# Optimization experiments

Measured on AMD Instinct MI355X. Metric: run time of the kernel, lower is better.

Reference implementation:

```python
import jax, jax.numpy as jnp
import numpy as np

D_MODEL = 1024
D_STATE = 16
D_CONV = 4
BATCH = 2
SEQ = 2048


def setup_inputs() -> dict:
    key = jax.random.key(0)
    ks = jax.random.split(key, 10)
    s = lambda fan_in: 1.0 / np.sqrt(fan_in)
    x = jax.random.normal(ks[0], (BATCH, SEQ, D_MODEL), dtype=jnp.float32)
    W_in = jax.random.normal(ks[1], (D_MODEL, 2 * D_MODEL), dtype=jnp.float32) * s(D_MODEL)
    conv_w = jax.random.normal(ks[2], (D_MODEL, D_CONV), dtype=jnp.float32) * s(D_CONV)
    conv_b = jax.random.normal(ks[3], (D_MODEL,), dtype=jnp.float32) * 0.01
    W_x = jax.random.normal(ks[4], (D_MODEL, 2 * D_STATE), dtype=jnp.float32) * s(D_MODEL)
    W_dt = jax.random.normal(ks[5], (D_MODEL, D_MODEL), dtype=jnp.float32) * s(D_MODEL)
    b_dt = jax.random.normal(ks[6], (D_MODEL,), dtype=jnp.float32) * 0.01
    A_log = jax.random.normal(ks[7], (D_MODEL,), dtype=jnp.float32) * 0.1
    D_param = jnp.ones((D_MODEL,), dtype=jnp.float32)
    W_out = jax.random.normal(ks[8], (D_MODEL, D_MODEL), dtype=jnp.float32) * s(D_MODEL)
    return {"x": x, "W_in": W_in, "conv_w": conv_w, "conv_b": conv_b,
            "W_x": W_x, "W_dt": W_dt, "b_dt": b_dt, "A_log": A_log,
            "D_param": D_param, "W_out": W_out}


def _selective_scan(x, A, dt, B, C):
    # x, dt: [b, l, d]; A: [d]; B, C: [b, l, n]
    b, l, d = x.shape
    n = B.shape[-1]
    h0 = jnp.zeros((b, d, n), dtype=x.dtype)

    def step(h, inp):
        x_t, dt_t, B_t, C_t = inp  # [b,d], [b,d], [b,n], [b,n]
        dA = jnp.exp(dt_t * A)[..., None]            # [b, d, 1]
        h = h * dA + x_t[..., None] * B_t[:, None, :]  # [b, d, n]
        y_t = jnp.einsum('bdn,bn->bd', h, C_t)
        return h, y_t

    xs = (jnp.swapaxes(x, 0, 1), jnp.swapaxes(dt, 0, 1),
          jnp.swapaxes(B, 0, 1), jnp.swapaxes(C, 0, 1))
    _, ys = jax.lax.scan(step, h0, xs)               # ys: [l, b, d]
    return jnp.swapaxes(ys, 0, 1)


def _forward(x, W_in, conv_w, conv_b, W_x, W_dt, b_dt, A_log, D_param, W_out):
    seq_len = x.shape[1]
    xz = x @ W_in                                     # [b, l, 2d]
    x_ssm, z = jnp.split(xz, 2, axis=-1)
    # causal depthwise conv (torch pads both sides then slices -> left pad only)
    xc = jnp.swapaxes(x_ssm, 1, 2)                    # [b, d, l]
    kernel = conv_w[:, None, :]                       # [d, 1, k]
    xc = jax.lax.conv_general_dilated(
        xc, kernel, window_strides=(1,), padding=[(D_CONV - 1, 0)],
        dimension_numbers=('NCH', 'OIH', 'NCH'), feature_group_count=D_MODEL)
    xc = xc + conv_b[None, :, None]
    x_ssm = jnp.swapaxes(xc, 1, 2)[:, :seq_len]       # [b, l, d]
    x_ssm = jax.nn.silu(x_ssm)
    A = -jnp.exp(A_log)
    dt = jax.nn.softplus(x_ssm @ W_dt + b_dt)
    BC = x_ssm @ W_x
    B, C = jnp.split(BC, 2, axis=-1)
    y = _selective_scan(x_ssm, A, dt, B, C)
    y = y + x_ssm * D_param
    y = y * jax.nn.silu(z)
    return y @ W_out


def reference(x, W_in, conv_w, conv_b, W_x, W_dt, b_dt, A_log, D_param, W_out):
    return _forward(x, W_in, conv_w, conv_b, W_x, W_dt, b_dt, A_log, D_param, W_out)
```

## Files before the change

### kernel.cpp

```cpp
#include <hip/hip_runtime.h>
#include <hip/hip_bf16.h>
#include <math.h>

#define D_MODEL 1024
#define D_STATE 16
#define D_CONV  4
#define BATCH   2
#define SEQ     2048
#define MROWS   (BATCH * SEQ)
#define CHUNK   32
#define NCHUNK  (SEQ / CHUNK)
#define BD      (BATCH * D_MODEL)

typedef __attribute__((ext_vector_type(8))) short bf16x8;
typedef __attribute__((ext_vector_type(4))) float f32x4;

__device__ __forceinline__ unsigned short f2bf(float f) {
    unsigned int u = __builtin_bit_cast(unsigned int, f);
    u = (u + 0x7fffu + ((u >> 16) & 1u)) >> 16;
    return (unsigned short)u;
}
__device__ __forceinline__ float bf2f(unsigned short u) {
    return __builtin_bit_cast(float, (unsigned int)u << 16);
}
__device__ __forceinline__ float softplus_f(float v) {
    return (v > 20.f) ? v : log1pf(expf(v));
}

__device__ __forceinline__ void gl2lds16(const unsigned short* g, unsigned short* l) {
    __builtin_amdgcn_global_load_lds(
        (__attribute__((address_space(1))) void*)(void*)g,
        (__attribute__((address_space(3))) void*)(void*)l, 16, 0, 0);
}

__global__ __launch_bounds__(256) void cvt_bf16(const float* __restrict__ src,
                                                unsigned short* __restrict__ dst) {
    const size_t i = ((size_t)blockIdx.x * 256 + threadIdx.x) * 8;
    const float4 v0 = *(const float4*)(src + i);
    const float4 v1 = *(const float4*)(src + i + 4);
    bf16x8 o;
    o[0] = (short)f2bf(v0.x); o[1] = (short)f2bf(v0.y);
    o[2] = (short)f2bf(v0.z); o[3] = (short)f2bf(v0.w);
    o[4] = (short)f2bf(v1.x); o[5] = (short)f2bf(v1.y);
    o[6] = (short)f2bf(v1.z); o[7] = (short)f2bf(v1.w);
    *(bf16x8*)(dst + i) = o;
}

__global__ __launch_bounds__(256) void wtrans(const float* __restrict__ W,
                                              unsigned short* __restrict__ Wt,
                                              int K, int N) {
    __shared__ float tile[32][33];
    const int n0 = blockIdx.x * 32, k0 = blockIdx.y * 32;
    const int tx = threadIdx.x & 31, ty = threadIdx.x >> 5;
#pragma unroll
    for (int r = 0; r < 4; ++r)
        tile[ty + r * 8][tx] = W[(size_t)(k0 + ty + r * 8) * N + n0 + tx];
    __syncthreads();
#pragma unroll
    for (int r = 0; r < 4; ++r)
        Wt[(size_t)(n0 + ty + r * 8) * K + k0 + tx] = f2bf(tile[tx][ty + r * 8]);
}

__global__ __launch_bounds__(256) void wx_stage(const float* __restrict__ Wx,
                                                unsigned short* __restrict__ Wt_cat) {
    const int idx = blockIdx.x * 256 + threadIdx.x;
    const int k = idx & 1023;
    const int n = idx >> 10;
    unsigned short v = 0;
    if (n < 32) v = f2bf(Wx[(size_t)k * 32 + n]);
    Wt_cat[(size_t)(1024 + n) * 1024 + k] = v;
}

template <int EPI>
__global__ __launch_bounds__(256) void gemm64(
        const unsigned short* __restrict__ A, const unsigned short* __restrict__ Bt,
        void* __restrict__ Cout, int N, int K,
        const float* __restrict__ bias, const float* __restrict__ alog,
        float* __restrict__ bc) {
    __shared__ unsigned short As[2][64 * 32];
    __shared__ unsigned short Bs[2][128 * 32];

    const int tid  = threadIdx.x;
    const int wave = tid >> 6, lane = tid & 63;
    const int q = lane >> 4, mr = lane & 15;
    const int m0 = blockIdx.y * 64, n0 = blockIdx.x * 128;

    f32x4 acc[4][2];
#pragma unroll
    for (int mi = 0; mi < 4; ++mi)
#pragma unroll
        for (int ni = 0; ni < 2; ++ni) acc[mi][ni] = {0.f, 0.f, 0.f, 0.f};

    const int kb = (tid & 3) * 8;
    const unsigned short* Ag  = A + (size_t)(m0 + (tid >> 2)) * K + kb;
    const unsigned short* Bg0 = Bt + (size_t)(n0 + (tid >> 2)) * K + kb;
    const unsigned short* Bg1 = Bt + (size_t)(n0 + ((tid + 256) >> 2)) * K + kb;
    const int sA = tid * 8, sB0 = tid * 8, sB1 = (tid + 256) * 8;

    const int NK = K >> 5;
    gl2lds16(Ag, As[0] + sA);
    gl2lds16(Bg0, Bs[0] + sB0);
    gl2lds16(Bg1, Bs[0] + sB1);

    for (int i = 0; i < NK; ++i) {
        __syncthreads();
        const int cur = i & 1, nxt = cur ^ 1;
        if (i + 1 < NK) {
            const int ko = (i + 1) * 32;
            gl2lds16(Ag + ko, As[nxt] + sA);
            gl2lds16(Bg0 + ko, Bs[nxt] + sB0);
            gl2lds16(Bg1 + ko, Bs[nxt] + sB1);
        }
        bf16x8 af[4], bfr[2];
#pragma unroll
        for (int mi = 0; mi < 4; ++mi)
            af[mi] = *(const bf16x8*)(As[cur] + (mi * 16 + mr) * 32 + q * 8);
#pragma unroll
        for (int ni = 0; ni < 2; ++ni)
            bfr[ni] = *(const bf16x8*)(Bs[cur] + (wave * 32 + ni * 16 + mr) * 32 + q * 8);
#pragma unroll
        for (int mi = 0; mi < 4; ++mi)
#pragma unroll
            for (int ni = 0; ni < 2; ++ni)
                acc[mi][ni] = __builtin_amdgcn_mfma_f32_16x16x32_bf16(
                    af[mi], bfr[ni], acc[mi][ni], 0, 0, 0);
    }

#pragma unroll
    for (int ni = 0; ni < 2; ++ni) {
        const int col = n0 + wave * 32 + ni * 16 + mr;
        float be = 0.f, al = 0.f;
        if (EPI == 3 && col < 1024) { be = bias[col]; al = alog[col]; }
#pragma unroll
        for (int mi = 0; mi < 4; ++mi) {
            const int row0 = m0 + mi * 16 + q * 4;
#pragma unroll
            for (int r = 0; r < 4; ++r) {
                float v = acc[mi][ni][r];
                const int row = row0 + r;
                if (EPI == 0) {
                    ((float*)Cout)[(size_t)row * N + col] = v;
                } else if (EPI == 2) {
                    ((unsigned short*)Cout)[(size_t)row * N + col] = f2bf(v);
                } else {
                    if (col < 1024) {
                        float dt = softplus_f(v + be);
                        ((unsigned short*)Cout)[(size_t)row * 1024 + col] =
                            f2bf(expf(dt * (-expf(al))));
                    } else if (col < 1056) {
                        bc[(size_t)row * 32 + (col - 1024)] = v;
                    }
                }
            }
        }
    }
}

__global__ __launch_bounds__(256) void conv_silu_kernel(
        const unsigned short* __restrict__ xz, const float* __restrict__ conv_w,
        const float* __restrict__ conv_b, unsigned short* __restrict__ xssm) {
    const int idx = blockIdx.x * 256 + threadIdx.x;
    const int d8 = idx & 127;
    const int bt = idx >> 7;
    const int t  = bt & (SEQ - 1);
    const int d  = d8 * 8;

    float4 w[8];
#pragma unroll
    for (int i = 0; i < 8; ++i) w[i] = *(const float4*)&conv_w[(d + i) * 4];

    float acc[8];
    {
        const float4 b0 = *(const float4*)&conv_b[d];
        const float4 b1 = *(const float4*)&conv_b[d + 4];
        acc[0] = b0.x; acc[1] = b0.y; acc[2] = b0.z; acc[3] = b0.w;
        acc[4] = b1.x; acc[5] = b1.y; acc[6] = b1.z; acc[7] = b1.w;
    }

#pragma unroll
    for (int j = 0; j < D_CONV; ++j) {
        const int tt = t - (D_CONV - 1) + j;
        if (tt < 0) continue;
        const bf16x8 xv = *(const bf16x8*)(&xz[((size_t)(bt - t + tt)) * 2048 + d]);
        const float wj[8] = {j == 0 ? w[0].x : j == 1 ? w[0].y : j == 2 ? w[0].z : w[0].w,
                             j == 0 ? w[1].x : j == 1 ? w[1].y : j == 2 ? w[1].z : w[1].w,
                             j == 0 ? w[2].x : j == 1 ? w[2].y : j == 2 ? w[2].z : w[2].w,
                             j == 0 ? w[3].x : j == 1 ? w[3].y : j == 2 ? w[3].z : w[3].w,
                             j == 0 ? w[4].x : j == 1 ? w[4].y : j == 2 ? w[4].z : w[4].w,
                             j == 0 ? w[5].x : j == 1 ? w[5].y : j == 2 ? w[5].z : w[5].w,
                             j == 0 ? w[6].x : j == 1 ? w[6].y : j == 2 ? w[6].z : w[6].w,
                             j == 0 ? w[7].x : j == 1 ? w[7].y : j == 2 ? w[7].z : w[7].w};
#pragma unroll
        for (int i = 0; i < 8; ++i)
            acc[i] += bf2f((unsigned short)xv[i]) * wj[i];
    }
    bf16x8 o;
#pragma unroll
    for (int i = 0; i < 8; ++i) {
        const float s = acc[i] / (1.f + expf(-acc[i]));
        o[i] = (short)f2bf(s);
    }
    *(bf16x8*)(&xssm[(size_t)bt * D_MODEL + d]) = o;
}

__global__ __launch_bounds__(256) void scan_pass1(
        const unsigned short* __restrict__ xssm, const unsigned short* __restrict__ dA16,
        const float* __restrict__ BCb,
        float* __restrict__ Sbuf, float* __restrict__ Pbuf) {
    const int ch = blockIdx.x, dg = blockIdx.y, b = blockIdx.z;
    const int tid = threadIdx.x;
    const int dd  = dg * 256 + tid;
    const int t0  = ch * CHUNK;

    __shared__ float Bs[CHUNK][16];
    if (tid < CHUNK * 4) {
        const int t = tid >> 2, j = (tid & 3) * 4;
        *(float4*)&Bs[t][j] = *(const float4*)&BCb[((size_t)b * SEQ + t0 + t) * 32 + j];
    }
    __syncthreads();

    const size_t base = ((size_t)b * SEQ + t0) * D_MODEL + dd;
    float h[16];
#pragma unroll
    for (int n = 0; n < 16; ++n) h[n] = 0.f;
    float P = 1.f;

    for (int g = 0; g < CHUNK; g += 8) {
        float dAr[8], xr[8];
#pragma unroll
        for (int p = 0; p < 8; ++p) {
            const size_t o = base + (size_t)(g + p) * D_MODEL;
            dAr[p] = bf2f(dA16[o]);
            xr[p]  = bf2f(xssm[o]);
        }
#pragma unroll
        for (int p = 0; p < 8; ++p) {
            const int t = g + p;
            const float dA = dAr[p], x = xr[p];
            P *= dA;
            const float4 B0 = *(const float4*)&Bs[t][0];
            const float4 B1 = *(const float4*)&Bs[t][4];
            const float4 B2 = *(const float4*)&Bs[t][8];
            const float4 B3 = *(const float4*)&Bs[t][12];
            h[0]  = h[0]  * dA + x * B0.x;  h[1]  = h[1]  * dA + x * B0.y;
            h[2]  = h[2]  * dA + x * B0.z;  h[3]  = h[3]  * dA + x * B0.w;
            h[4]  = h[4]  * dA + x * B1.x;  h[5]  = h[5]  * dA + x * B1.y;
            h[6]  = h[6]  * dA + x * B1.z;  h[7]  = h[7]  * dA + x * B1.w;
            h[8]  = h[8]  * dA + x * B2.x;  h[9]  = h[9]  * dA + x * B2.y;
            h[10] = h[10] * dA + x * B2.z;  h[11] = h[11] * dA + x * B2.w;
            h[12] = h[12] * dA + x * B3.x;  h[13] = h[13] * dA + x * B3.y;
            h[14] = h[14] * dA + x * B3.z;  h[15] = h[15] * dA + x * B3.w;
        }
    }

    const int dn = b * D_MODEL + dd;
    const size_t so = ((size_t)ch * BD + dn) * 16;
#pragma unroll
    for (int n = 0; n < 16; n += 4)
        *(float4*)&Sbuf[so + n] = make_float4(h[n], h[n + 1], h[n + 2], h[n + 3]);
    Pbuf[(size_t)ch * BD + dn] = P;
}

__global__ __launch_bounds__(128) void scan_mid(
        const float* __restrict__ Sbuf, const float* __restrict__ Pbuf,
        float* __restrict__ Hin) {
    const int idx = blockIdx.x * 128 + threadIdx.x;
    const int n   = idx & 15;
    const int dn  = idx >> 4;

    float h = 0.f;
    for (int ch = 0; ch < NCHUNK; ++ch) {
        const size_t s = ((size_t)ch * BD + dn) * 16 + n;
        Hin[s] = h;
        h = Pbuf[(size_t)ch * BD + dn] * h + Sbuf[s];
    }
}

__global__ __launch_bounds__(256) void scan_pass2(
        const unsigned short* __restrict__ xssm, const unsigned short* __restrict__ dA16,
        const float* __restrict__ BCb, const unsigned short* __restrict__ xz,
        const float* __restrict__ Dp, const float* __restrict__ Hin,
        unsigned short* __restrict__ ybuf) {
    const int ch = blockIdx.x, dg = blockIdx.y, b = blockIdx.z;
    const int tid = threadIdx.x;
    const int dd  = dg * 256 + tid;
    const int t0  = ch * CHUNK;

    __shared__ float BCs[CHUNK][32];
    {
        const int t = tid >> 3, j = (tid & 7) * 4;
        *(float4*)&BCs[t][j] = *(const float4*)&BCb[((size_t)b * SEQ + t0 + t) * 32 + j];
    }
    __syncthreads();

    const float Dpv = Dp[dd];
    const size_t base  = ((size_t)b * SEQ + t0) * D_MODEL + dd;
    const size_t baseZ = ((size_t)b * SEQ + t0) * 2048 + D_MODEL + dd;

    float h[16];
    const int dn = b * D_MODEL + dd;
    const size_t ho = ((size_t)ch * BD + dn) * 16;
#pragma unroll
    for (int n = 0; n < 16; n += 4) {
        const float4 hv = *(const float4*)&Hin[ho + n];
        h[n] = hv.x; h[n + 1] = hv.y; h[n + 2] = hv.z; h[n + 3] = hv.w;
    }

    for (int g = 0; g < CHUNK; g += 8) {
        float dAr[8], xr[8], zr[8];
#pragma unroll
        for (int p = 0; p < 8; ++p) {
            const size_t o = base + (size_t)(g + p) * D_MODEL;
            dAr[p] = bf2f(dA16[o]);
            xr[p]  = bf2f(xssm[o]);
            zr[p]  = bf2f(xz[baseZ + (size_t)(g + p) * 2048]);
        }
#pragma unroll
        for (int p = 0; p < 8; ++p) {
            const int t = g + p;
            const float dA = dAr[p], x = xr[p];
            const float4 B0 = *(const float4*)&BCs[t][0];
            const float4 B1 = *(const float4*)&BCs[t][4];
            const float4 B2 = *(const float4*)&BCs[t][8];
            const float4 B3 = *(const float4*)&BCs[t][12];
            const float4 C0 = *(const float4*)&BCs[t][16];
            const float4 C1 = *(const float4*)&BCs[t][20];
            const float4 C2 = *(const float4*)&BCs[t][24];
            const float4 C3 = *(const float4*)&BCs[t][28];
            float y = 0.f;
            h[0]  = h[0]  * dA + x * B0.x;  y += h[0]  * C0.x;
            h[1]  = h[1]  * dA + x * B0.y;  y += h[1]  * C0.y;
            h[2]  = h[2]  * dA + x * B0.z;  y += h[2]  * C0.z;
            h[3]  = h[3]  * dA + x * B0.w;  y += h[3]  * C0.w;
            h[4]  = h[4]  * dA + x * B1.x;  y += h[4]  * C1.x;
            h[5]  = h[5]  * dA + x * B1.y;  y += h[5]  * C1.y;
            h[6]  = h[6]  * dA + x * B1.z;  y += h[6]  * C1.z;
            h[7]  = h[7]  * dA + x * B1.w;  y += h[7]  * C1.w;
            h[8]  = h[8]  * dA + x * B2.x;  y += h[8]  * C2.x;
            h[9]  = h[9]  * dA + x * B2.y;  y += h[9]  * C2.y;
            h[10] = h[10] * dA + x * B2.z;  y += h[10] * C2.z;
            h[11] = h[11] * dA + x * B2.w;  y += h[11] * C2.w;
            h[12] = h[12] * dA + x * B3.x;  y += h[12] * C3.x;
            h[13] = h[13] * dA + x * B3.y;  y += h[13] * C3.y;
            h[14] = h[14] * dA + x * B3.z;  y += h[14] * C3.z;
            h[15] = h[15] * dA + x * B3.w;  y += h[15] * C3.w;

            const float zv = zr[p];
            const float sz = zv / (1.f + expf(-zv));
            ybuf[base + (size_t)t * D_MODEL] = f2bf((y + x * Dpv) * sz);
        }
    }
}

extern "C" void kernel_launch(void* const* d_in, const int* in_sizes, int n_in,
                              void* d_out, int out_size, void* d_ws, size_t ws_size,
                              hipStream_t stream) {
    const float* x       = (const float*)d_in[0];
    const float* W_in    = (const float*)d_in[1];
    const float* conv_w  = (const float*)d_in[2];
    const float* conv_b  = (const float*)d_in[3];
    const float* W_x     = (const float*)d_in[4];
    const float* W_dt    = (const float*)d_in[5];
    const float* b_dt    = (const float*)d_in[6];
    const float* A_log   = (const float*)d_in[7];
    const float* D_param = (const float*)d_in[8];
    const float* W_out   = (const float*)d_in[9];
    float* out = (float*)d_out;
    char* ws   = (char*)d_ws;

    unsigned short* xz_bf   = (unsigned short*)(ws + 0);
    unsigned short* xssm_bf = (unsigned short*)(ws + 16777216);
    unsigned short* dAb16   = (unsigned short*)(ws + 25165824);
    float*          BCb     = (float*)(ws + 41943040);
    unsigned short* ybuf_bf = (unsigned short*)(ws + 42467328);
    unsigned short* xb      = (unsigned short*)(ws + 50855936);
    unsigned short* Wt_in   = (unsigned short*)(ws + 59244544);
    unsigned short* Wt_cat  = (unsigned short*)(ws + 63438848);
    unsigned short* Wt_out  = (unsigned short*)(ws + 65798144);
    float*          Sbuf    = (float*)(ws + 67895296);
    float*          Pbuf    = (float*)(ws + 76283904);
    float*          Hin     = (float*)(ws + 76808192);

    cvt_bf16<<<MROWS * D_MODEL / (256 * 8), 256, 0, stream>>>(x, xb);
    wtrans<<<dim3(2048 / 32, 1024 / 32), 256, 0, stream>>>(W_in, Wt_in, 1024, 2048);
    wtrans<<<dim3(1024 / 32, 1024 / 32), 256, 0, stream>>>(W_dt, Wt_cat, 1024, 1024);
    wx_stage<<<(128 * 1024) / 256, 256, 0, stream>>>(W_x, Wt_cat);
    wtrans<<<dim3(1024 / 32, 1024 / 32), 256, 0, stream>>>(W_out, Wt_out, 1024, 1024);

    gemm64<2><<<dim3(2048 / 128, MROWS / 64), 256, 0, stream>>>(
        xb, Wt_in, xz_bf, 2048, D_MODEL, nullptr, nullptr, nullptr);
    conv_silu_kernel<<<(MROWS * 128) / 256, 256, 0, stream>>>(xz_bf, conv_w, conv_b, xssm_bf);
    gemm64<3><<<dim3(1152 / 128, MROWS / 64), 256, 0, stream>>>(
        xssm_bf, Wt_cat, dAb16, 1152, D_MODEL, b_dt, A_log, BCb);
    scan_pass1<<<dim3(NCHUNK, D_MODEL / 256, BATCH), 256, 0, stream>>>(
        xssm_bf, dAb16, BCb, Sbuf, Pbuf);
    scan_mid<<<(BD * 16) / 128, 128, 0, stream>>>(Sbuf, Pbuf, Hin);
    scan_pass2<<<dim3(NCHUNK, D_MODEL / 256, BATCH), 256, 0, stream>>>(
        xssm_bf, dAb16, BCb, xz_bf, D_param, Hin, ybuf_bf);
    gemm64<0><<<dim3(1024 / 128, MROWS / 64), 256, 0, stream>>>(
        ybuf_bf, Wt_out, out, D_MODEL, D_MODEL, nullptr, nullptr, nullptr);
}
```

Before: 253.9 us.

## Merge preprocessing kernels into one launch and deepen GEMM K-tile to 64

Five conversion and transpose launches (x to bf16, three weight transposes, W_x staging) become one prepass kernel that dispatches by block index, which removes launch overhead and the gaps between launches. The bf16 GEMM now stages a K step of 64 per iteration, as two 32-wide sub-tiles, instead of 32. This halves the number of barriers and loop iterations and issues more loads per pipeline stage. The cost is twice the LDS use per block (48KB), which may lower occupancy.

```diff
diff --git a/kernel.cpp b/kernel.cpp
--- a/kernel.cpp
+++ b/kernel.cpp
@@ -33,42 +33,53 @@
         (__attribute__((address_space(3))) void*)(void*)l, 16, 0, 0);
 }
 
-__global__ __launch_bounds__(256) void cvt_bf16(const float* __restrict__ src,
-                                                unsigned short* __restrict__ dst) {
-    const size_t i = ((size_t)blockIdx.x * 256 + threadIdx.x) * 8;
-    const float4 v0 = *(const float4*)(src + i);
-    const float4 v1 = *(const float4*)(src + i + 4);
-    bf16x8 o;
-    o[0] = (short)f2bf(v0.x); o[1] = (short)f2bf(v0.y);
-    o[2] = (short)f2bf(v0.z); o[3] = (short)f2bf(v0.w);
-    o[4] = (short)f2bf(v1.x); o[5] = (short)f2bf(v1.y);
-    o[6] = (short)f2bf(v1.z); o[7] = (short)f2bf(v1.w);
-    *(bf16x8*)(dst + i) = o;
-}
-
-__global__ __launch_bounds__(256) void wtrans(const float* __restrict__ W,
-                                              unsigned short* __restrict__ Wt,
-                                              int K, int N) {
+__global__ __launch_bounds__(256) void prepass(
+        const float* __restrict__ x, unsigned short* __restrict__ xb,
+        const float* __restrict__ W_in, unsigned short* __restrict__ Wt_in,
+        const float* __restrict__ W_dt, unsigned short* __restrict__ Wt_cat,
+        const float* __restrict__ W_out, unsigned short* __restrict__ Wt_out,
+        const float* __restrict__ Wx) {
     __shared__ float tile[32][33];
-    const int n0 = blockIdx.x * 32, k0 = blockIdx.y * 32;
-    const int tx = threadIdx.x & 31, ty = threadIdx.x >> 5;
-#pragma unroll
-    for (int r = 0; r < 4; ++r)
-        tile[ty + r * 8][tx] = W[(size_t)(k0 + ty + r * 8) * N + n0 + tx];
-    __syncthreads();
-#pragma unroll
-    for (int r = 0; r < 4; ++r)
-        Wt[(size_t)(n0 + ty + r * 8) * K + k0 + tx] = f2bf(tile[tx][ty + r * 8]);
-}
-
-__global__ __launch_bounds__(256) void wx_stage(const float* __restrict__ Wx,
-                                                unsigned short* __restrict__ Wt_cat) {
-    const int idx = blockIdx.x * 256 + threadIdx.x;
-    const int k = idx & 1023;
-    const int n = idx >> 10;
-    unsigned short v = 0;
-    if (n < 32) v = f2bf(Wx[(size_t)k * 32 + n]);
-    Wt_cat[(size_t)(1024 + n) * 1024 + k] = v;
+    const int blk = blockIdx.x;
+    const int tid = threadIdx.x;
+
+    if (blk < 2048) {
+        const size_t i = ((size_t)blk * 256 + tid) * 8;
+        const float4 v0 = *(const float4*)(x + i);
+        const float4 v1 = *(const float4*)(x + i + 4);
+        bf16x8 o;
+        o[0] = (short)f2bf(v0.x); o[1] = (short)f2bf(v0.y);
+        o[2] = (short)f2bf(v0.z); o[3] = (short)f2bf(v0.w);
+        o[4] = (short)f2bf(v1.x); o[5] = (short)f2bf(v1.y);
+        o[6] = (short)f2bf(v1.z); o[7] = (short)f2bf(v1.w);
+        *(bf16x8*)(xb + i) = o;
+        return;
+    }
+    if (blk < 2048 + 2048 + 1024 + 1024) {
+        const float* W; unsigned short* Wt; int N, b;
+        if (blk < 4096)      { W = W_in;  Wt = Wt_in;  N = 2048; b = blk - 2048; }
+        else if (blk < 5120) { W = W_dt;  Wt = Wt_cat; N = 1024; b = blk - 4096; }
+        else                 { W = W_out; Wt = Wt_out; N = 1024; b = blk - 5120; }
+        const int nx = N / 32;
+        const int n0 = (b % nx) * 32, k0 = (b / nx) * 32;
+        const int tx = tid & 31, ty = tid >> 5;
+#pragma unroll
+        for (int r = 0; r < 4; ++r)
+            tile[ty + r * 8][tx] = W[(size_t)(k0 + ty + r * 8) * N + n0 + tx];
+        __syncthreads();
+#pragma unroll
+        for (int r = 0; r < 4; ++r)
+            Wt[(size_t)(n0 + ty + r * 8) * 1024 + k0 + tx] = f2bf(tile[tx][ty + r * 8]);
+        return;
+    }
+    {
+        const int idx = (blk - 6144) * 256 + tid;
+        const int k = idx & 1023;
+        const int n = idx >> 10;
+        unsigned short v = 0;
+        if (n < 32) v = f2bf(Wx[(size_t)k * 32 + n]);
+        Wt_cat[(size_t)(1024 + n) * 1024 + k] = v;
+    }
 }
 
 template <int EPI>
@@ -77,8 +88,8 @@
         void* __restrict__ Cout, int N, int K,
         const float* __restrict__ bias, const float* __restrict__ alog,
         float* __restrict__ bc) {
-    __shared__ unsigned short As[2][64 * 32];
-    __shared__ unsigned short Bs[2][128 * 32];
+    __shared__ unsigned short As[2][2 * 2048];
+    __shared__ unsigned short Bs[2][2 * 4096];
 
     const int tid  = threadIdx.x;
     const int wave = tid >> 6, lane = tid & 63;
@@ -92,38 +103,52 @@
         for (int ni = 0; ni < 2; ++ni) acc[mi][ni] = {0.f, 0.f, 0.f, 0.f};
 
     const int kb = (tid & 3) * 8;
-    const unsigned short* Ag  = A + (size_t)(m0 + (tid >> 2)) * K + kb;
-    const unsigned short* Bg0 = Bt + (size_t)(n0 + (tid >> 2)) * K + kb;
-    const unsigned short* Bg1 = Bt + (size_t)(n0 + ((tid + 256) >> 2)) * K + kb;
-    const int sA = tid * 8, sB0 = tid * 8, sB1 = (tid + 256) * 8;
-
-    const int NK = K >> 5;
-    gl2lds16(Ag, As[0] + sA);
-    gl2lds16(Bg0, Bs[0] + sB0);
-    gl2lds16(Bg1, Bs[0] + sB1);
+    const int rA = tid >> 2;
+    const unsigned short* AgL = A + (size_t)(m0 + rA) * K + kb;
+    const unsigned short* AgH = AgL + 32;
+    const unsigned short* Bg0L = Bt + (size_t)(n0 + rA) * K + kb;
+    const unsigned short* Bg0H = Bg0L + 32;
+    const unsigned short* Bg1L = Bt + (size_t)(n0 + 64 + rA) * K + kb;
+    const unsigned short* Bg1H = Bg1L + 32;
+    const int sT = tid * 8;
+
+    const int NK = K >> 6;
+    gl2lds16(AgL, As[0] + sT);
+    gl2lds16(AgH, As[0] + 2048 + sT);
+    gl2lds16(Bg0L, Bs[0] + sT);
+    gl2lds16(Bg1L, Bs[0] + 2048 + sT);
+    gl2lds16(Bg0H, Bs[0] + 4096 + sT);
+    gl2lds16(Bg1H, Bs[0] + 6144 + sT);
 
     for (int i = 0; i < NK; ++i) {
         __syncthreads();
         const int cur = i & 1, nxt = cur ^ 1;
         if (i + 1 < NK) {
-            const int ko = (i + 1) * 32;
-            gl2lds16(Ag + ko, As[nxt] + sA);
-            gl2lds16(Bg0 + ko, Bs[nxt] + sB0);
-            gl2lds16(Bg1 + ko, Bs[nxt] + sB1);
-        }
-        bf16x8 af[4], bfr[2];
-#pragma unroll
-        for (int mi = 0; mi < 4; ++mi)
-            af[mi] = *(const bf16x8*)(As[cur] + (mi * 16 + mr) * 32 + q * 8);
-#pragma unroll
-        for (int ni = 0; ni < 2; ++ni)
-            bfr[ni] = *(const bf16x8*)(Bs[cur] + (wave * 32 + ni * 16 + mr) * 32 + q * 8);
-#pragma unroll
-        for (int mi = 0; mi < 4; ++mi)
+            const int ko = (i + 1) * 64;
+            gl2lds16(AgL + ko, As[nxt] + sT);
+            gl2lds16(AgH + ko, As[nxt] + 2048 + sT);
+            gl2lds16(Bg0L + ko, Bs[nxt] + sT);
+            gl2lds16(Bg1L + ko, Bs[nxt] + 2048 + sT);
+            gl2lds16(Bg0H + ko, Bs[nxt] + 4096 + sT);
+            gl2lds16(Bg1H + ko, Bs[nxt] + 6144 + sT);
+        }
+#pragma unroll
+        for (int ks = 0; ks < 2; ++ks) {
+            bf16x8 af[4], bfr[2];
+#pragma unroll
+            for (int mi = 0; mi < 4; ++mi)
+                af[mi] = *(const bf16x8*)(As[cur] + ks * 2048 + (mi * 16 + mr) * 32 + q * 8);
 #pragma unroll
             for (int ni = 0; ni < 2; ++ni)
-                acc[mi][ni] = __builtin_amdgcn_mfma_f32_16x16x32_bf16(
-                    af[mi], bfr[ni], acc[mi][ni], 0, 0, 0);
+                bfr[ni] = *(const bf16x8*)(Bs[cur] + ks * 4096 +
+                                           (wave * 32 + ni * 16 + mr) * 32 + q * 8);
+#pragma unroll
+            for (int mi = 0; mi < 4; ++mi)
+#pragma unroll
+                for (int ni = 0; ni < 2; ++ni)
+                    acc[mi][ni] = __builtin_amdgcn_mfma_f32_16x16x32_bf16(
+                        af[mi], bfr[ni], acc[mi][ni], 0, 0, 0);
+        }
     }
 
 #pragma unroll
@@ -381,11 +406,8 @@
     float*          Pbuf    = (float*)(ws + 76283904);
     float*          Hin     = (float*)(ws + 76808192);
 
-    cvt_bf16<<<MROWS * D_MODEL / (256 * 8), 256, 0, stream>>>(x, xb);
-    wtrans<<<dim3(2048 / 32, 1024 / 32), 256, 0, stream>>>(W_in, Wt_in, 1024, 2048);
-    wtrans<<<dim3(1024 / 32, 1024 / 32), 256, 0, stream>>>(W_dt, Wt_cat, 1024, 1024);
-    wx_stage<<<(128 * 1024) / 256, 256, 0, stream>>>(W_x, Wt_cat);
-    wtrans<<<dim3(1024 / 32, 1024 / 32), 256, 0, stream>>>(W_out, Wt_out, 1024, 1024);
+    prepass<<<2048 + 2048 + 1024 + 1024 + 512, 256, 0, stream>>>(
+        x, xb, W_in, Wt_in, W_dt, Wt_cat, W_out, Wt_out, W_x);
 
     gemm64<2><<<dim3(2048 / 128, MROWS / 64), 256, 0, stream>>>(
         xb, Wt_in, xz_bf, 2048, D_MODEL, nullptr, nullptr, nullptr);
```

Result: faster. 245.8 us (-3.2%).
